# Kernel optimization log

Hardware: AMD Instinct MI355X
Metric: run time of the kernel (lower is better)

## Reference

```python
import jax, jax.numpy as jnp
import numpy as np

N_EMBED = 384
NUM_HEADS = 6
HEAD_SIZE = N_EMBED // NUM_HEADS  # 64
B, T = 8, 2048


def setup_inputs() -> dict:
    key = jax.random.key(0)
    ks = jax.random.split(key, 8)
    s = 1.0 / np.sqrt(N_EMBED)
    query = jax.random.normal(ks[0], (B, T, N_EMBED), dtype=jnp.float32)
    key_t = jax.random.normal(ks[1], (B, T, N_EMBED), dtype=jnp.float32)
    value = jax.random.normal(ks[2], (B, T, N_EMBED), dtype=jnp.float32)
    # causal-style mask, broadcastable over (B, H)
    mask = jnp.tril(jnp.ones((T, T), dtype=jnp.int32))[None, None]
    Wk = jax.random.normal(ks[3], (N_EMBED, N_EMBED), dtype=jnp.float32) * s
    Wq = jax.random.normal(ks[4], (N_EMBED, N_EMBED), dtype=jnp.float32) * s
    Wv = jax.random.normal(ks[5], (N_EMBED, N_EMBED), dtype=jnp.float32) * s
    Wproj = jax.random.normal(ks[6], (N_EMBED, N_EMBED), dtype=jnp.float32) * s
    bproj = jnp.zeros((N_EMBED,), dtype=jnp.float32)
    return {"query": query, "key": key_t, "value": value, "mask": mask,
            "Wk": Wk, "Wq": Wq, "Wv": Wv, "Wproj": Wproj, "bproj": bproj}


def _split_heads(x):
    b, t, c = x.shape
    return x.reshape(b, t, NUM_HEADS, c // NUM_HEADS).transpose(0, 2, 1, 3)  # [B,H,T,D]


def reference(query, key, value, mask, Wk, Wq, Wv, Wproj, bproj):
    b, t, c = query.shape
    # NOTE: source swaps names: k = key_proj(query), q = query_proj(key)
    k = _split_heads(query @ Wk.T)
    q = _split_heads(key @ Wq.T)
    v = _split_heads(value @ Wv.T)
    # scale by full C (not head_size), as in the source
    wei = jnp.einsum("bhqd,bhkd->bhqk", q, k) * (c ** -0.5)
    # masked_fill with 0 BEFORE softmax (faithful to source)
    wei = jnp.where(mask == 0, jnp.float32(0.0), wei)
    wei = jax.nn.softmax(wei, axis=-1)
    out = jnp.einsum("bhqk,bhkd->bhqd", wei, v)
    out = out.transpose(0, 2, 1, 3).reshape(b, t, c)
    out = out @ Wproj.T + bproj  # dropout is identity at inference
    return out
```

## Files before the change

### kernel.cpp

```cpp
#include <hip/hip_runtime.h>
#include <hip/hip_bf16.h>


#define TT 2048
#define CC 384
#define HH 6
#define DD 64
#define SCALE 0.05103103630798288f

typedef __bf16 bf16x8 __attribute__((ext_vector_type(8)));
typedef __bf16 bf16x4 __attribute__((ext_vector_type(4)));
typedef float f32x4 __attribute__((ext_vector_type(4)));

__device__ __forceinline__ int swz(int row, int byteInRow) {
    return row * 128 + (byteInRow ^ ((row & 7) << 4));
}

__global__ __launch_bounds__(256) void qkv_proj_kernel(
    const float* __restrict__ query, const float* __restrict__ key,
    const float* __restrict__ value, const float* __restrict__ Wk,
    const float* __restrict__ Wq, const float* __restrict__ Wv,
    __bf16* __restrict__ Kb, __bf16* __restrict__ Qb, __bf16* __restrict__ VTb)
{
    __shared__ __align__(16) char smem[49152];

    const int tid = threadIdx.x;
    const int wid = tid >> 6, lane = tid & 63;
    const int lrow = lane & 15, g = lane >> 4;
    const int pid = blockIdx.z;
    const int m0 = blockIdx.x * 128, n0 = blockIdx.y * 64;
    const float* X = (pid == 0) ? query : ((pid == 1) ? key : value);
    const float* W = (pid == 0) ? Wk : ((pid == 1) ? Wq : Wv);

    const int xrow = tid >> 4, xcol = (tid & 15) * 4;
    const float* xp = X + (size_t)(m0 + xrow) * CC + xcol;
    const float* wp = W + (size_t)(n0 + (tid >> 4)) * CC + xcol;

    f32x4 xr[8], wr[4];

    f32x4 acc[2][4];
#pragma unroll
    for (int i = 0; i < 2; ++i)
#pragma unroll
        for (int j = 0; j < 4; ++j) acc[i][j] = (f32x4){0.f, 0.f, 0.f, 0.f};

#pragma unroll
    for (int i = 0; i < 8; ++i) xr[i] = *(const f32x4*)(xp + (size_t)i * 16 * CC);
#pragma unroll
    for (int i = 0; i < 4; ++i) wr[i] = *(const f32x4*)(wp + (size_t)i * 16 * CC);
    {
        char* Xd = smem;
        char* Wd = smem + 32768;
#pragma unroll
        for (int i = 0; i < 8; ++i) {
            bf16x4 hh;
            hh[0] = (__bf16)xr[i][0]; hh[1] = (__bf16)xr[i][1];
            hh[2] = (__bf16)xr[i][2]; hh[3] = (__bf16)xr[i][3];
            *(bf16x4*)(Xd + swz(xrow + i * 16, xcol * 2)) = hh;
        }
#pragma unroll
        for (int i = 0; i < 4; ++i) {
            bf16x4 hh;
            hh[0] = (__bf16)wr[i][0]; hh[1] = (__bf16)wr[i][1];
            hh[2] = (__bf16)wr[i][2]; hh[3] = (__bf16)wr[i][3];
            *(bf16x4*)(Wd + swz((tid >> 4) + i * 16, xcol * 2)) = hh;
        }
    }
    __syncthreads();

    int cur = 0;
    for (int kk = 0; kk < 6; ++kk) {
        if (kk < 5) {
            const int k0 = (kk + 1) * 64;
#pragma unroll
            for (int i = 0; i < 8; ++i) xr[i] = *(const f32x4*)(xp + (size_t)i * 16 * CC + k0);
#pragma unroll
            for (int i = 0; i < 4; ++i) wr[i] = *(const f32x4*)(wp + (size_t)i * 16 * CC + k0);
        }
        const char* Xs = smem + cur * 16384;
        const char* Ws = smem + 32768 + cur * 8192;

        __builtin_amdgcn_s_setprio(1);
        if (pid < 2) {
#pragma unroll
            for (int kc = 0; kc < 2; ++kc) {
                int kb = kc * 64 + g * 16;
                bf16x8 a0 = *(bf16x8*)(Xs + swz(wid * 32 + lrow, kb));
                bf16x8 a1 = *(bf16x8*)(Xs + swz(wid * 32 + 16 + lrow, kb));
#pragma unroll
                for (int nf = 0; nf < 4; ++nf) {
                    bf16x8 b = *(bf16x8*)(Ws + swz(nf * 16 + lrow, kb));
                    acc[0][nf] = __builtin_amdgcn_mfma_f32_16x16x32_bf16(a0, b, acc[0][nf], 0, 0, 0);
                    acc[1][nf] = __builtin_amdgcn_mfma_f32_16x16x32_bf16(a1, b, acc[1][nf], 0, 0, 0);
                }
            }
        } else {
#pragma unroll
            for (int kc = 0; kc < 2; ++kc) {
                int kb = kc * 64 + g * 16;
                bf16x8 b0 = *(bf16x8*)(Xs + swz(wid * 32 + lrow, kb));
                bf16x8 b1 = *(bf16x8*)(Xs + swz(wid * 32 + 16 + lrow, kb));
#pragma unroll
                for (int nf = 0; nf < 4; ++nf) {
                    bf16x8 a = *(bf16x8*)(Ws + swz(nf * 16 + lrow, kb));
                    acc[0][nf] = __builtin_amdgcn_mfma_f32_16x16x32_bf16(a, b0, acc[0][nf], 0, 0, 0);
                    acc[1][nf] = __builtin_amdgcn_mfma_f32_16x16x32_bf16(a, b1, acc[1][nf], 0, 0, 0);
                }
            }
        }
        __builtin_amdgcn_s_setprio(0);

        if (kk < 5) {
            char* Xd = smem + (cur ^ 1) * 16384;
            char* Wd = smem + 32768 + (cur ^ 1) * 8192;
#pragma unroll
            for (int i = 0; i < 8; ++i) {
                bf16x4 hh;
                hh[0] = (__bf16)xr[i][0]; hh[1] = (__bf16)xr[i][1];
                hh[2] = (__bf16)xr[i][2]; hh[3] = (__bf16)xr[i][3];
                *(bf16x4*)(Xd + swz(xrow + i * 16, xcol * 2)) = hh;
            }
#pragma unroll
            for (int i = 0; i < 4; ++i) {
                bf16x4 hh;
                hh[0] = (__bf16)wr[i][0]; hh[1] = (__bf16)wr[i][1];
                hh[2] = (__bf16)wr[i][2]; hh[3] = (__bf16)wr[i][3];
                *(bf16x4*)(Wd + swz((tid >> 4) + i * 16, xcol * 2)) = hh;
            }
        }
        __syncthreads();
        cur ^= 1;
    }

    if (pid < 2) {
        __bf16* out = (pid == 0) ? Kb : Qb;
#pragma unroll
        for (int mf = 0; mf < 2; ++mf)
#pragma unroll
            for (int nf = 0; nf < 4; ++nf)
#pragma unroll
                for (int r = 0; r < 4; ++r) {
                    int m = m0 + wid * 32 + mf * 16 + g * 4 + r;
                    int n = n0 + nf * 16 + lrow;
                    int b = m >> 11, t = m & 2047, h = n >> 6, d = n & 63;
                    out[((size_t)(b * HH + h) * TT + t) * DD + d] = (__bf16)acc[mf][nf][r];
                }
    } else {
#pragma unroll
        for (int mf = 0; mf < 2; ++mf)
#pragma unroll
            for (int nf = 0; nf < 4; ++nf)
#pragma unroll
                for (int r = 0; r < 4; ++r) {
                    int n = n0 + nf * 16 + g * 4 + r;
                    int m = m0 + wid * 32 + mf * 16 + lrow;
                    int b = m >> 11, t = m & 2047, h = n >> 6, d = n & 63;
                    VTb[((size_t)(b * HH + h) * DD + d) * TT + t] = (__bf16)acc[mf][nf][r];
                }
    }
}

__global__ __launch_bounds__(256) void suffix_kernel(
    const __bf16* __restrict__ VTb, float* __restrict__ Ssuf)
{
    __shared__ float tsum[4][32];
    const int bh = blockIdx.x;
    const int tid = threadIdx.x, wid = tid >> 6, lane = tid & 63;

#pragma unroll
    for (int it = 0; it < 4; ++it) {
        const int dr = blockIdx.y * 16 + wid * 4 + it;
        const __bf16* src = VTb + (size_t)(bh * DD + dr) * TT;
#pragma unroll
        for (int step = 0; step < 4; ++step) {
            bf16x8 v = *(const bf16x8*)(src + step * 512 + lane * 8);
            float sacc = 0.f;
#pragma unroll
            for (int i = 0; i < 8; ++i) sacc += (float)v[i];
            sacc += __shfl_xor(sacc, 1);
            sacc += __shfl_xor(sacc, 2);
            sacc += __shfl_xor(sacc, 4);
            if ((lane & 7) == 0) tsum[wid][step * 8 + (lane >> 3)] = sacc;
        }
        float s2 = 0.f;
        for (int j = 0; j < 32; ++j) {
            float tv = tsum[wid][j];
            if (j >= lane) s2 += tv;
        }
        if (lane <= 32) Ssuf[(size_t)(bh * 33 + lane) * 64 + dr] = s2;
    }
}

__global__ __launch_bounds__(256) void attn_kernel(
    const __bf16* __restrict__ Qb, const __bf16* __restrict__ Kb,
    const __bf16* __restrict__ VTb, const float* __restrict__ Ssuf,
    __bf16* __restrict__ attn)
{
    __shared__ __align__(16) char smem[32768];
    const int tid = threadIdx.x;
    const int wid = tid >> 6, lane = tid & 63;
    const int lrow = lane & 15, g = lane >> 4;

    const int bh = blockIdx.y;
    const int qt = (int)gridDim.x - 1 - (int)blockIdx.x;
    const int q0 = qt * 64;

    const __bf16* qp = Qb + ((size_t)bh * TT + q0 + wid * 16 + lrow) * DD + g * 8;
    const bf16x8 qb0 = *(const bf16x8*)qp;
    const bf16x8 qb1 = *(const bf16x8*)(qp + 32);

    const int r0 = tid >> 3;
    const int c8 = (tid & 7) * 8;
    const __bf16* kbase = Kb + (size_t)bh * TT * DD;
    const __bf16* vbase = VTb + (size_t)bh * DD * TT;

    bf16x8 kr0, kr1, vr0, vr1;

    f32x4 o[4];
#pragma unroll
    for (int ds = 0; ds < 4; ++ds) o[ds] = (f32x4){0.f, 0.f, 0.f, 0.f};
    float z = 0.f;

    kr0 = *(const bf16x8*)(kbase + (size_t)r0 * DD + c8);
    kr1 = *(const bf16x8*)(kbase + (size_t)(r0 + 32) * DD + c8);
    vr0 = *(const bf16x8*)(vbase + (size_t)r0 * TT + c8);
    vr1 = *(const bf16x8*)(vbase + (size_t)(r0 + 32) * TT + c8);
    {
        char* Kd = smem;
        char* Vd = smem + 16384;
        *(bf16x8*)(Kd + swz(r0, c8 * 2)) = kr0;
        *(bf16x8*)(Kd + swz(r0 + 32, c8 * 2)) = kr1;
        *(bf16x8*)(Vd + swz(r0, c8 * 2)) = vr0;
        *(bf16x8*)(Vd + swz(r0 + 32, c8 * 2)) = vr1;
    }
    __syncthreads();

    int cur = 0;
    for (int kt = 0; kt <= qt; ++kt) {
        if (kt < qt) {
            const int n0 = (kt + 1) * 64;
            kr0 = *(const bf16x8*)(kbase + (size_t)(n0 + r0) * DD + c8);
            kr1 = *(const bf16x8*)(kbase + (size_t)(n0 + r0 + 32) * DD + c8);
            vr0 = *(const bf16x8*)(vbase + (size_t)r0 * TT + n0 + c8);
            vr1 = *(const bf16x8*)(vbase + (size_t)(r0 + 32) * TT + n0 + c8);
        }
        const char* Kc = smem + cur * 8192;
        const char* Vc = smem + 16384 + cur * 8192;

        f32x4 st[4];
#pragma unroll
        for (int j16 = 0; j16 < 4; ++j16) st[j16] = (f32x4){0.f, 0.f, 0.f, 0.f};
        __builtin_amdgcn_s_setprio(1);
#pragma unroll
        for (int kc = 0; kc < 2; ++kc) {
            bf16x8 qf = kc ? qb1 : qb0;
#pragma unroll
            for (int j16 = 0; j16 < 4; ++j16) {
                bf16x8 kf = *(bf16x8*)(Kc + swz(j16 * 16 + lrow, kc * 64 + g * 16));
                st[j16] = __builtin_amdgcn_mfma_f32_16x16x32_bf16(kf, qf, st[j16], 0, 0, 0);
            }
        }
        __builtin_amdgcn_s_setprio(0);

        const bool dm = (kt == qt);
        bf16x8 pb0, pb1;
#pragma unroll
        for (int j16 = 0; j16 < 4; ++j16) {
#pragma unroll
            for (int r = 0; r < 4; ++r) {
                float p;
                if (dm && (j16 * 16 + g * 4 + r > wid * 16 + lrow)) p = 1.0f;
                else p = __expf(st[j16][r] * SCALE);
                z += p;
                if (j16 < 2) pb0[(j16 & 1) * 4 + r] = (__bf16)p;
                else         pb1[(j16 & 1) * 4 + r] = (__bf16)p;
            }
        }

        __builtin_amdgcn_s_setprio(1);
#pragma unroll
        for (int kc = 0; kc < 2; ++kc) {
            bf16x8 pf = kc ? pb1 : pb0;
#pragma unroll
            for (int ds = 0; ds < 4; ++ds) {
                union { bf16x8 v8; bf16x4 h[2]; } vf;
                vf.h[0] = *(bf16x4*)(Vc + swz(ds * 16 + lrow, kc * 64 + 8 * g));
                vf.h[1] = *(bf16x4*)(Vc + swz(ds * 16 + lrow, kc * 64 + 8 * g + 32));
                o[ds] = __builtin_amdgcn_mfma_f32_16x16x32_bf16(vf.v8, pf, o[ds], 0, 0, 0);
            }
        }
        __builtin_amdgcn_s_setprio(0);

        if (kt < qt) {
            char* Kd = smem + (cur ^ 1) * 8192;
            char* Vd = smem + 16384 + (cur ^ 1) * 8192;
            *(bf16x8*)(Kd + swz(r0, c8 * 2)) = kr0;
            *(bf16x8*)(Kd + swz(r0 + 32, c8 * 2)) = kr1;
            *(bf16x8*)(Vd + swz(r0, c8 * 2)) = vr0;
            *(bf16x8*)(Vd + swz(r0 + 32, c8 * 2)) = vr1;
        }
        __syncthreads();
        cur ^= 1;
    }

    z += __shfl_xor(z, 16);
    z += __shfl_xor(z, 32);
    z += (float)(TT - (qt + 1) * 64);
    const float inv = 1.0f / z;

    const float* suf = Ssuf + ((size_t)bh * 33 + qt + 1) * 64;
    const int b = bh / HH, h = bh % HH;
    const int t = q0 + wid * 16 + lrow;
    __bf16* orow = attn + ((size_t)(b * TT + t)) * CC + h * DD;
#pragma unroll
    for (int ds = 0; ds < 4; ++ds) {
        f32x4 sv = *(const f32x4*)(suf + ds * 16 + g * 4);
        bf16x4 w;
#pragma unroll
        for (int r = 0; r < 4; ++r) w[r] = (__bf16)((o[ds][r] + sv[r]) * inv);
        *(bf16x4*)(orow + ds * 16 + g * 4) = w;
    }
}

__global__ __launch_bounds__(256) void out_proj_kernel(
    const __bf16* __restrict__ A, const float* __restrict__ W,
    const float* __restrict__ bias, float* __restrict__ out)
{
    __shared__ __align__(16) char smem[49152];
    const int tid = threadIdx.x;
    const int wid = tid >> 6, lane = tid & 63;
    const int lrow = lane & 15, g = lane >> 4;
    const int m0 = blockIdx.x * 128, n0 = blockIdx.y * 64;

    const int arow = tid >> 3, ac8 = (tid & 7) * 8;
    const __bf16* ap = A + (size_t)(m0 + arow) * CC + ac8;
    const int wrow = tid >> 4, wcol = (tid & 15) * 4;
    const float* wp = W + (size_t)(n0 + wrow) * CC + wcol;

    bf16x8 ar[4];
    f32x4 wr[4];

    f32x4 acc[2][4];
#pragma unroll
    for (int i = 0; i < 2; ++i)
#pragma unroll
        for (int j = 0; j < 4; ++j) acc[i][j] = (f32x4){0.f, 0.f, 0.f, 0.f};

#pragma unroll
    for (int i = 0; i < 4; ++i) ar[i] = *(const bf16x8*)(ap + (size_t)i * 32 * CC);
#pragma unroll
    for (int i = 0; i < 4; ++i) wr[i] = *(const f32x4*)(wp + (size_t)i * 16 * CC);
    {
        char* Ad = smem;
        char* Wd = smem + 32768;
#pragma unroll
        for (int i = 0; i < 4; ++i)
            *(bf16x8*)(Ad + swz(arow + i * 32, ac8 * 2)) = ar[i];
#pragma unroll
        for (int i = 0; i < 4; ++i) {
            bf16x4 hh;
            hh[0] = (__bf16)wr[i][0]; hh[1] = (__bf16)wr[i][1];
            hh[2] = (__bf16)wr[i][2]; hh[3] = (__bf16)wr[i][3];
            *(bf16x4*)(Wd + swz(wrow + i * 16, wcol * 2)) = hh;
        }
    }
    __syncthreads();

    int cur = 0;
    for (int kk = 0; kk < 6; ++kk) {
        if (kk < 5) {
            const int k0 = (kk + 1) * 64;
#pragma unroll
            for (int i = 0; i < 4; ++i) ar[i] = *(const bf16x8*)(ap + (size_t)i * 32 * CC + k0);
#pragma unroll
            for (int i = 0; i < 4; ++i) wr[i] = *(const f32x4*)(wp + (size_t)i * 16 * CC + k0);
        }
        const char* Xs = smem + cur * 16384;
        const char* Ws = smem + 32768 + cur * 8192;

        __builtin_amdgcn_s_setprio(1);
#pragma unroll
        for (int kc = 0; kc < 2; ++kc) {
            int kb = kc * 64 + g * 16;
            bf16x8 a0 = *(bf16x8*)(Xs + swz(wid * 32 + lrow, kb));
            bf16x8 a1 = *(bf16x8*)(Xs + swz(wid * 32 + 16 + lrow, kb));
#pragma unroll
            for (int nf = 0; nf < 4; ++nf) {
                bf16x8 b = *(bf16x8*)(Ws + swz(nf * 16 + lrow, kb));
                acc[0][nf] = __builtin_amdgcn_mfma_f32_16x16x32_bf16(a0, b, acc[0][nf], 0, 0, 0);
                acc[1][nf] = __builtin_amdgcn_mfma_f32_16x16x32_bf16(a1, b, acc[1][nf], 0, 0, 0);
            }
        }
        __builtin_amdgcn_s_setprio(0);

        if (kk < 5) {
            char* Ad = smem + (cur ^ 1) * 16384;
            char* Wd = smem + 32768 + (cur ^ 1) * 8192;
#pragma unroll
            for (int i = 0; i < 4; ++i)
                *(bf16x8*)(Ad + swz(arow + i * 32, ac8 * 2)) = ar[i];
#pragma unroll
            for (int i = 0; i < 4; ++i) {
                bf16x4 hh;
                hh[0] = (__bf16)wr[i][0]; hh[1] = (__bf16)wr[i][1];
                hh[2] = (__bf16)wr[i][2]; hh[3] = (__bf16)wr[i][3];
                *(bf16x4*)(Wd + swz(wrow + i * 16, wcol * 2)) = hh;
            }
        }
        __syncthreads();
        cur ^= 1;
    }

#pragma unroll
    for (int nf = 0; nf < 4; ++nf) {
        float bv = bias[n0 + nf * 16 + lrow];
#pragma unroll
        for (int mf = 0; mf < 2; ++mf)
#pragma unroll
            for (int r = 0; r < 4; ++r) {
                int m = m0 + wid * 32 + mf * 16 + g * 4 + r;
                out[(size_t)m * CC + n0 + nf * 16 + lrow] = acc[mf][nf][r] + bv;
            }
    }
}

extern "C" void kernel_launch(void* const* d_in, const int* in_sizes, int n_in,
                              void* d_out, int out_size, void* d_ws, size_t ws_size,
                              hipStream_t stream)
{
    (void)in_sizes; (void)n_in; (void)out_size; (void)ws_size;
    const float* query = (const float*)d_in[0];
    const float* key   = (const float*)d_in[1];
    const float* value = (const float*)d_in[2];
    const float* Wk    = (const float*)d_in[4];
    const float* Wq    = (const float*)d_in[5];
    const float* Wv    = (const float*)d_in[6];
    const float* Wproj = (const float*)d_in[7];
    const float* bproj = (const float*)d_in[8];
    float* out = (float*)d_out;

    char* ws = (char*)d_ws;
    const size_t SZ = 12582912;
    __bf16* Qb   = (__bf16*)(ws);
    __bf16* Kb   = (__bf16*)(ws + SZ);
    __bf16* VTb  = (__bf16*)(ws + 2 * SZ);
    __bf16* Ab   = (__bf16*)(ws + 3 * SZ);
    float*  Ssuf = (float*)(ws + 4 * SZ);

    qkv_proj_kernel<<<dim3(128, 6, 3), 256, 0, stream>>>(query, key, value,
                                                         Wk, Wq, Wv, Kb, Qb, VTb);
    suffix_kernel<<<dim3(48, 4), 256, 0, stream>>>(VTb, Ssuf);
    attn_kernel<<<dim3(32, 48), 256, 0, stream>>>(Qb, Kb, VTb, Ssuf, Ab);
    out_proj_kernel<<<dim3(128, 6), 256, 0, stream>>>(Ab, Wproj, bproj, out);
}
```

Baseline: 278.3 us.

## Enlarge attention query tile to 128 rows and remap grid for XCD locality

The attention kernel now gives each block 128 query rows instead of 64, with each wave computing two 16-row MFMA fragments. Every K/V tile staged in shared memory therefore feeds twice as much compute, halving global and LDS staging traffic per query. The grid becomes a 1D launch of 768 blocks whose index is remapped so consecutive blocks spread over batch-heads and run the longest causal tiles first. The cost is more accumulator registers, fewer blocks, and diagonal masking now spanning two key tiles per query tile.

```diff
diff --git a/kernel.cpp b/kernel.cpp
--- a/kernel.cpp
+++ b/kernel.cpp
@@ -201,13 +201,20 @@
     const int wid = tid >> 6, lane = tid & 63;
     const int lrow = lane & 15, g = lane >> 4;
 
-    const int bh = blockIdx.y;
-    const int qt = (int)gridDim.x - 1 - (int)blockIdx.x;
-    const int q0 = qt * 64;
-
-    const __bf16* qp = Qb + ((size_t)bh * TT + q0 + wid * 16 + lrow) * DD + g * 8;
-    const bf16x8 qb0 = *(const bf16x8*)qp;
-    const bf16x8 qb1 = *(const bf16x8*)(qp + 32);
+    const int i = blockIdx.x;
+    const int j = i >> 3;
+    const int bh = (i & 7) * 6 + (j >> 4);
+    const int Qt = 15 - (j & 15);
+    const int q0 = Qt * 128;
+    const int nkt = 2 * Qt + 2;
+
+    const int qloc = wid * 32 + lrow;
+    const __bf16* qp = Qb + ((size_t)bh * TT + q0 + qloc) * DD + g * 8;
+    bf16x8 qb[2][2];
+    qb[0][0] = *(const bf16x8*)(qp);
+    qb[0][1] = *(const bf16x8*)(qp + 32);
+    qb[1][0] = *(const bf16x8*)(qp + 16 * DD);
+    qb[1][1] = *(const bf16x8*)(qp + 16 * DD + 32);
 
     const int r0 = tid >> 3;
     const int c8 = (tid & 7) * 8;
@@ -216,10 +223,12 @@
 
     bf16x8 kr0, kr1, vr0, vr1;
 
-    f32x4 o[4];
-#pragma unroll
-    for (int ds = 0; ds < 4; ++ds) o[ds] = (f32x4){0.f, 0.f, 0.f, 0.f};
-    float z = 0.f;
+    f32x4 o[2][4];
+#pragma unroll
+    for (int mf = 0; mf < 2; ++mf)
+#pragma unroll
+        for (int ds = 0; ds < 4; ++ds) o[mf][ds] = (f32x4){0.f, 0.f, 0.f, 0.f};
+    float z0 = 0.f, z1 = 0.f;
 
     kr0 = *(const bf16x8*)(kbase + (size_t)r0 * DD + c8);
     kr1 = *(const bf16x8*)(kbase + (size_t)(r0 + 32) * DD + c8);
@@ -236,8 +245,8 @@
     __syncthreads();
 
     int cur = 0;
-    for (int kt = 0; kt <= qt; ++kt) {
-        if (kt < qt) {
+    for (int kt = 0; kt < nkt; ++kt) {
+        if (kt + 1 < nkt) {
             const int n0 = (kt + 1) * 64;
             kr0 = *(const bf16x8*)(kbase + (size_t)(n0 + r0) * DD + c8);
             kr1 = *(const bf16x8*)(kbase + (size_t)(n0 + r0 + 32) * DD + c8);
@@ -246,52 +255,58 @@
         }
         const char* Kc = smem + cur * 8192;
         const char* Vc = smem + 16384 + cur * 8192;
-
-        f32x4 st[4];
-#pragma unroll
-        for (int j16 = 0; j16 < 4; ++j16) st[j16] = (f32x4){0.f, 0.f, 0.f, 0.f};
-        __builtin_amdgcn_s_setprio(1);
-#pragma unroll
-        for (int kc = 0; kc < 2; ++kc) {
-            bf16x8 qf = kc ? qb1 : qb0;
+        const bool dm = (kt >= 2 * Qt);
+
+#pragma unroll
+        for (int mf = 0; mf < 2; ++mf) {
+            f32x4 st[4];
+#pragma unroll
+            for (int j16 = 0; j16 < 4; ++j16) st[j16] = (f32x4){0.f, 0.f, 0.f, 0.f};
+            __builtin_amdgcn_s_setprio(1);
+#pragma unroll
+            for (int kc = 0; kc < 2; ++kc) {
+                bf16x8 qf = qb[mf][kc];
+#pragma unroll
+                for (int j16 = 0; j16 < 4; ++j16) {
+                    bf16x8 kf = *(bf16x8*)(Kc + swz(j16 * 16 + lrow, kc * 64 + g * 16));
+                    st[j16] = __builtin_amdgcn_mfma_f32_16x16x32_bf16(kf, qf, st[j16], 0, 0, 0);
+                }
+            }
+            __builtin_amdgcn_s_setprio(0);
+
+            const int qg = q0 + qloc + mf * 16;
+            bf16x8 pb0, pb1;
+            float zz = 0.f;
 #pragma unroll
             for (int j16 = 0; j16 < 4; ++j16) {
-                bf16x8 kf = *(bf16x8*)(Kc + swz(j16 * 16 + lrow, kc * 64 + g * 16));
-                st[j16] = __builtin_amdgcn_mfma_f32_16x16x32_bf16(kf, qf, st[j16], 0, 0, 0);
-            }
-        }
-        __builtin_amdgcn_s_setprio(0);
-
-        const bool dm = (kt == qt);
-        bf16x8 pb0, pb1;
-#pragma unroll
-        for (int j16 = 0; j16 < 4; ++j16) {
-#pragma unroll
-            for (int r = 0; r < 4; ++r) {
-                float p;
-                if (dm && (j16 * 16 + g * 4 + r > wid * 16 + lrow)) p = 1.0f;
-                else p = __expf(st[j16][r] * SCALE);
-                z += p;
-                if (j16 < 2) pb0[(j16 & 1) * 4 + r] = (__bf16)p;
-                else         pb1[(j16 & 1) * 4 + r] = (__bf16)p;
-            }
-        }
-
-        __builtin_amdgcn_s_setprio(1);
-#pragma unroll
-        for (int kc = 0; kc < 2; ++kc) {
-            bf16x8 pf = kc ? pb1 : pb0;
-#pragma unroll
-            for (int ds = 0; ds < 4; ++ds) {
-                union { bf16x8 v8; bf16x4 h[2]; } vf;
-                vf.h[0] = *(bf16x4*)(Vc + swz(ds * 16 + lrow, kc * 64 + 8 * g));
-                vf.h[1] = *(bf16x4*)(Vc + swz(ds * 16 + lrow, kc * 64 + 8 * g + 32));
-                o[ds] = __builtin_amdgcn_mfma_f32_16x16x32_bf16(vf.v8, pf, o[ds], 0, 0, 0);
-            }
-        }
-        __builtin_amdgcn_s_setprio(0);
-
-        if (kt < qt) {
+#pragma unroll
+                for (int r = 0; r < 4; ++r) {
+                    float p;
+                    if (dm && (kt * 64 + j16 * 16 + g * 4 + r > qg)) p = 1.0f;
+                    else p = __expf(st[j16][r] * SCALE);
+                    zz += p;
+                    if (j16 < 2) pb0[(j16 & 1) * 4 + r] = (__bf16)p;
+                    else         pb1[(j16 & 1) * 4 + r] = (__bf16)p;
+                }
+            }
+            if (mf == 0) z0 += zz; else z1 += zz;
+
+            __builtin_amdgcn_s_setprio(1);
+#pragma unroll
+            for (int kc = 0; kc < 2; ++kc) {
+                bf16x8 pf = kc ? pb1 : pb0;
+#pragma unroll
+                for (int ds = 0; ds < 4; ++ds) {
+                    union { bf16x8 v8; bf16x4 h[2]; } vf;
+                    vf.h[0] = *(bf16x4*)(Vc + swz(ds * 16 + lrow, kc * 64 + 8 * g));
+                    vf.h[1] = *(bf16x4*)(Vc + swz(ds * 16 + lrow, kc * 64 + 8 * g + 32));
+                    o[mf][ds] = __builtin_amdgcn_mfma_f32_16x16x32_bf16(vf.v8, pf, o[mf][ds], 0, 0, 0);
+                }
+            }
+            __builtin_amdgcn_s_setprio(0);
+        }
+
+        if (kt + 1 < nkt) {
             char* Kd = smem + (cur ^ 1) * 8192;
             char* Vd = smem + 16384 + (cur ^ 1) * 8192;
             *(bf16x8*)(Kd + swz(r0, c8 * 2)) = kr0;
@@ -303,22 +318,27 @@
         cur ^= 1;
     }
 
-    z += __shfl_xor(z, 16);
-    z += __shfl_xor(z, 32);
-    z += (float)(TT - (qt + 1) * 64);
-    const float inv = 1.0f / z;
-
-    const float* suf = Ssuf + ((size_t)bh * 33 + qt + 1) * 64;
+    const float fut = (float)(TT - nkt * 64);
+    z0 += __shfl_xor(z0, 16); z0 += __shfl_xor(z0, 32);
+    z1 += __shfl_xor(z1, 16); z1 += __shfl_xor(z1, 32);
+    const float inv0 = 1.0f / (z0 + fut);
+    const float inv1 = 1.0f / (z1 + fut);
+
+    const float* suf = Ssuf + ((size_t)bh * 33 + nkt) * 64;
     const int b = bh / HH, h = bh % HH;
-    const int t = q0 + wid * 16 + lrow;
-    __bf16* orow = attn + ((size_t)(b * TT + t)) * CC + h * DD;
-#pragma unroll
-    for (int ds = 0; ds < 4; ++ds) {
-        f32x4 sv = *(const f32x4*)(suf + ds * 16 + g * 4);
-        bf16x4 w;
-#pragma unroll
-        for (int r = 0; r < 4; ++r) w[r] = (__bf16)((o[ds][r] + sv[r]) * inv);
-        *(bf16x4*)(orow + ds * 16 + g * 4) = w;
+#pragma unroll
+    for (int mf = 0; mf < 2; ++mf) {
+        const int t = q0 + qloc + mf * 16;
+        const float inv = mf ? inv1 : inv0;
+        __bf16* orow = attn + ((size_t)(b * TT + t)) * CC + h * DD;
+#pragma unroll
+        for (int ds = 0; ds < 4; ++ds) {
+            f32x4 sv = *(const f32x4*)(suf + ds * 16 + g * 4);
+            bf16x4 w;
+#pragma unroll
+            for (int r = 0; r < 4; ++r) w[r] = (__bf16)((o[mf][ds][r] + sv[r]) * inv);
+            *(bf16x4*)(orow + ds * 16 + g * 4) = w;
+        }
     }
 }
 
@@ -450,6 +470,6 @@
     qkv_proj_kernel<<<dim3(128, 6, 3), 256, 0, stream>>>(query, key, value,
                                                          Wk, Wq, Wv, Kb, Qb, VTb);
     suffix_kernel<<<dim3(48, 4), 256, 0, stream>>>(VTb, Ssuf);
-    attn_kernel<<<dim3(32, 48), 256, 0, stream>>>(Qb, Kb, VTb, Ssuf, Ab);
+    attn_kernel<<<dim3(768), 256, 0, stream>>>(Qb, Kb, VTb, Ssuf, Ab);
     out_proj_kernel<<<dim3(128, 6), 256, 0, stream>>>(Ab, Wproj, bproj, out);
 }
```

Measured after the change: 274.2 us. No clear change (-1.5%).
